# Performance work log

Measured on AMD Instinct MI355X. Metric: run time of the kernel, lower is better.

Reference implementation:

```python
import jax, jax.numpy as jnp
import numpy as np

N = 50000    # nodes
R = 3        # relations
E = 600000   # edges per relation
IN, HID, OUT = 128, 64, 64


def setup_inputs() -> dict:
    key = jax.random.key(0)
    k = jax.random.split(key, 5)
    x = jax.random.normal(k[0], (N, IN), dtype=jnp.float32)
    src = jax.random.randint(k[1], (R, E), 0, N, dtype=jnp.int32)
    dst = jax.random.randint(k[2], (R, E), 0, N, dtype=jnp.int32)
    # glorot-ish init like dgl.nn.GraphConv weight; bias init zeros
    W1 = jax.random.normal(k[3], (R, IN, HID), dtype=jnp.float32) * (IN ** -0.5)
    b1 = jnp.zeros((R, HID), dtype=jnp.float32)
    W2 = jax.random.normal(k[4], (R, HID, OUT), dtype=jnp.float32) * (HID ** -0.5)
    b2 = jnp.zeros((R, OUT), dtype=jnp.float32)
    return {"x": x, "W1": W1, "b1": b1, "W2": W2, "b2": b2, "src": src, "dst": dst}


def _graph_conv(x, src, dst, W, b):
    """dgl.nn.GraphConv with norm='both', single relation.
    x: [N, Fin]; src/dst: [E] int; W: [Fin, Fout]; b: [Fout].
    """
    n = x.shape[0]
    ones = jnp.ones(src.shape[0], dtype=x.dtype)
    out_deg = jax.ops.segment_sum(ones, src, num_segments=n)
    h = x * (jnp.maximum(out_deg, 1.0) ** -0.5)[:, None]   # src-side norm
    if W.shape[0] > W.shape[1]:
        # mult W first, then aggregate (fewer flops per edge)
        h = h @ W
        agg = jax.ops.segment_sum(h[src], dst, num_segments=n)  # [N, Fout]
    else:
        agg = jax.ops.segment_sum(h[src], dst, num_segments=n) @ W
    in_deg = jax.ops.segment_sum(ones, dst, num_segments=n)
    return agg * (jnp.maximum(in_deg, 1.0) ** -0.5)[:, None] + b


def _hetero_conv(x, src, dst, W, b):
    # HeteroGraphConv(aggregate='sum'): run each relation's GraphConv, sum results.
    per_rel = jax.vmap(_graph_conv, in_axes=(None, 0, 0, 0, 0))(x, src, dst, W, b)
    return per_rel.sum(axis=0)  # [N, Fout]


def reference(x, W1, b1, W2, b2, src, dst):
    h = jax.nn.relu(_hetero_conv(x, src, dst, W1, b1))
    return _hetero_conv(h, src, dst, W2, b2)
```

## Files before the change

kernel.cpp:

```cpp
#include <hip/hip_runtime.h>

#define NODES 50000
#define RELS  3
#define NEDGE 600000
#define FIN   128
#define FHID  64
#define FOUT  64
#define SEGS  (RELS * NODES)
#define NBLK  ((SEGS + 255) / 256)

#define HC     96
#define HCHUNK (NEDGE / HC)
#define HBYTES NODES
#define HWORDS (HBYTES / 4)

#define BS     250
#define NBUK   200
#define NBUKT  (RELS * NBUK)
#define CAPLOG 12
#define CAP    (1 << CAPLOG)
#define BCH    192
#define BCHUNK (NEDGE / BCH)

typedef _Float16 half8 __attribute__((ext_vector_type(8)));
typedef float   floatx4 __attribute__((ext_vector_type(4)));

__global__ __launch_bounds__(1024) void hist_kernel(const int* __restrict__ src,
                                                    const int* __restrict__ dst,
                                                    unsigned int* __restrict__ slab32,
                                                    int* __restrict__ bcur) {
    __shared__ unsigned int bins[HWORDS];
    int chunk = blockIdx.x, job = blockIdx.y;
    if (chunk == 0 && job == 0 && threadIdx.x < NBUKT) bcur[threadIdx.x] = 0;
    const int* arr = (job < 3 ? src + (size_t)job * NEDGE
                              : dst + (size_t)(job - 3) * NEDGE) + (size_t)chunk * HCHUNK;
    for (int w = threadIdx.x; w < HWORDS; w += 1024) bins[w] = 0u;
    __syncthreads();
    for (int i = threadIdx.x; i < HCHUNK; i += 1024) {
        int v = arr[i];
        atomicAdd(&bins[v >> 2], 1u << ((v & 3) * 8));
    }
    __syncthreads();
    unsigned int* out = slab32 + ((size_t)(job * HC + chunk)) * HWORDS;
    for (int w = threadIdx.x; w < HWORDS; w += 1024) out[w] = bins[w];
}

__global__ __launch_bounds__(512) void bucketize_kernel(const int* __restrict__ src,
                                                        const int* __restrict__ dst,
                                                        int* __restrict__ bcur,
                                                        unsigned int* __restrict__ rec) {
    __shared__ unsigned int stage[BCHUNK];
    __shared__ int bh[NBUK], bbase[NBUK], blc[NBUK];
    int chunk = blockIdx.x, r = blockIdx.y;
    for (int i = threadIdx.x; i < NBUK; i += 512) { bh[i] = 0; blc[i] = 0; }
    __syncthreads();
    size_t ebase = (size_t)r * NEDGE + (size_t)chunk * BCHUNK;
    for (int i = threadIdx.x; i < BCHUNK; i += 512) {
        int d = dst[ebase + i], s = src[ebase + i];
        int b = d / BS;
        int dl = d - b * BS;
        stage[i] = ((unsigned)s << 16) | ((unsigned)b << 8) | (unsigned)dl;
        atomicAdd(&bh[b], 1);
    }
    __syncthreads();
    for (int i = threadIdx.x; i < NBUK; i += 512)
        bbase[i] = atomicAdd(&bcur[r * NBUK + i], bh[i]);
    __syncthreads();
    for (int i = threadIdx.x; i < BCHUNK; i += 512) {
        unsigned u = stage[i];
        int b = (u >> 8) & 255;
        int slot = bbase[b] + atomicAdd(&blc[b], 1);
        rec[(((size_t)r * NBUK + b) << CAPLOG) + slot] = u;
    }
}

__global__ __launch_bounds__(256) void degnorm_kernel(const unsigned char* __restrict__ slab8,
                                                      int* __restrict__ idI,
                                                      float* __restrict__ outnorm,
                                                      float* __restrict__ innorm,
                                                      const float* __restrict__ W1,
                                                      const float* __restrict__ W2,
                                                      _Float16* __restrict__ W1t,
                                                      _Float16* __restrict__ W2t) {
    int gid = blockIdx.x * 256 + threadIdx.x;
    if (gid < 6 * NODES) {
        int j = gid / NODES, b = gid - j * NODES;
        size_t base = (size_t)j * HC * HBYTES + b;
        int sum = 0;
#pragma unroll 4
        for (int c = 0; c < HC; ++c) sum += slab8[base + (size_t)c * HBYTES];
        float nrm = rsqrtf(fmaxf((float)sum, 1.0f));
        if (j < 3) {
            outnorm[j * NODES + b] = nrm;
        } else {
            idI[(j - 3) * NODES + b] = sum;
            innorm[(j - 3) * NODES + b] = nrm;
        }
        return;
    }
    int g2 = gid - 6 * NODES;
    if (g2 < RELS * FIN * FHID) {
        int r = g2 / (FIN * FHID);
        int rem = g2 - r * FIN * FHID;
        int k = rem / FHID, j = rem - k * FHID;
        W1t[((size_t)r * FHID + j) * FIN + k] = (_Float16)W1[g2];
        return;
    }
    int g3 = g2 - RELS * FIN * FHID;
    if (g3 < RELS * FHID * FOUT) {
        int r = g3 / (FHID * FOUT);
        int rem = g3 - r * FHID * FOUT;
        int k = rem / FOUT, j = rem - k * FOUT;
        W2t[((size_t)r * FOUT + j) * FHID + k] = (_Float16)W2[g3];
    }
}

__global__ __launch_bounds__(256) void scan_sums_kernel(const int* __restrict__ idI,
                                                        int* __restrict__ partials) {
    __shared__ int s[256];
    int i = blockIdx.x * 256 + threadIdx.x;
    s[threadIdx.x] = (i < SEGS) ? idI[i] : 0;
    __syncthreads();
    for (int off = 128; off > 0; off >>= 1) {
        if (threadIdx.x < off) s[threadIdx.x] += s[threadIdx.x + off];
        __syncthreads();
    }
    if (threadIdx.x == 0) partials[blockIdx.x] = s[0];
}

__global__ __launch_bounds__(256) void scan_write_kernel(const int* __restrict__ idI,
                                                         const int* __restrict__ partials,
                                                         int* __restrict__ offs) {
    __shared__ int sp[1024];
    __shared__ int s[256];
    int tid = threadIdx.x;
    for (int i = tid; i < 1024; i += 256) sp[i] = (i < NBLK) ? partials[i] : 0;
    __syncthreads();
    for (int off = 1; off < 1024; off <<= 1) {
        int v[4];
#pragma unroll
        for (int k = 0; k < 4; ++k) { int i = tid + k * 256; v[k] = (i >= off) ? sp[i - off] : 0; }
        __syncthreads();
#pragma unroll
        for (int k = 0; k < 4; ++k) sp[tid + k * 256] += v[k];
        __syncthreads();
    }
    int bpre = (blockIdx.x == 0) ? 0 : sp[blockIdx.x - 1];
    int i = blockIdx.x * 256 + tid;
    int v = (i < SEGS) ? idI[i] : 0;
    s[tid] = v;
    __syncthreads();
    for (int off = 1; off < 256; off <<= 1) {
        int t = s[tid];
        int add = (tid >= off) ? s[tid - off] : 0;
        __syncthreads();
        s[tid] = t + add;
        __syncthreads();
    }
    if (i < SEGS) offs[i] = bpre + (s[tid] - v);
}

__global__ __launch_bounds__(512) void fillbkt_kernel(const unsigned int* __restrict__ rec,
                                                      const int* __restrict__ bcur,
                                                      const int* __restrict__ offs,
                                                      unsigned short* __restrict__ edge_src) {
    __shared__ int obase[BS];
    __shared__ int lcur[BS];
    int b = blockIdx.x, r = blockIdx.y;
    int segbase = r * NODES + b * BS;
    for (int i = threadIdx.x; i < BS; i += 512) {
        obase[i] = offs[segbase + i];
        lcur[i] = 0;
    }
    __syncthreads();
    int n = bcur[r * NBUK + b];
    const unsigned int* rb = rec + (((size_t)r * NBUK + b) << CAPLOG);
    for (int i = threadIdx.x; i < n; i += 512) {
        unsigned u = rb[i];
        int dl = u & 255;
        int pos = obase[dl] + atomicAdd(&lcur[dl], 1);
        edge_src[pos] = (unsigned short)(u >> 16);
    }
}

__global__ __launch_bounds__(256, 4) void gemm1_kernel(const float* __restrict__ x,
                                                       const _Float16* __restrict__ W1t,
                                                       const float* __restrict__ outnorm,
                                                       _Float16* __restrict__ h) {
    int lane = threadIdx.x & 63;
    int wv   = threadIdx.x >> 6;
    int m = lane & 15, quad = lane >> 4;
    int n0 = (blockIdx.x * 4 + wv) * 16;
    if (n0 + 16 > NODES) n0 = NODES - 16;
    const float* xrow = x + (size_t)(n0 + m) * FIN + quad * 8;

    floatx4 acc[12];
#pragma unroll
    for (int t = 0; t < 12; ++t) acc[t] = (floatx4){0.f, 0.f, 0.f, 0.f};

#pragma unroll 1
    for (int ks = 0; ks < 4; ++ks) {
        float4 xa = *(const float4*)(xrow + ks * 32);
        float4 xb = *(const float4*)(xrow + ks * 32 + 4);
        half8 a;
        a[0] = (_Float16)xa.x; a[1] = (_Float16)xa.y;
        a[2] = (_Float16)xa.z; a[3] = (_Float16)xa.w;
        a[4] = (_Float16)xb.x; a[5] = (_Float16)xb.y;
        a[6] = (_Float16)xb.z; a[7] = (_Float16)xb.w;
#pragma unroll
        for (int jt = 0; jt < 12; ++jt) {
            const _Float16* bp = W1t + ((size_t)jt * 16 + m) * FIN + ks * 32 + quad * 8;
            half8 b = *(const half8*)bp;
            acc[jt] = __builtin_amdgcn_mfma_f32_16x16x32_f16(a, b, acc[jt], 0, 0, 0);
        }
    }

#pragma unroll
    for (int jt = 0; jt < 12; ++jt) {
        int r = jt >> 2;
        int j = (jt & 3) * 16 + m;
        _Float16* hb = h + (size_t)r * NODES * FHID;
        const float* on = outnorm + r * NODES;
#pragma unroll
        for (int reg = 0; reg < 4; ++reg) {
            int node = n0 + quad * 4 + reg;
            hb[(size_t)node * FHID + j] = (_Float16)(acc[jt][reg] * on[node]);
        }
    }
}

__device__ __forceinline__ void seg_sum8(const _Float16* __restrict__ hb,
                                         const unsigned short* __restrict__ es,
                                         int o, int c, int q, float* __restrict__ s) {
#pragma unroll
    for (int i = 0; i < 8; ++i) s[i] = 0.f;
    int t = 0;
    for (; t + 4 <= c; t += 4) {
        int i0 = es[o + t], i1 = es[o + t + 1], i2 = es[o + t + 2], i3 = es[o + t + 3];
        half8 v0 = *(const half8*)(hb + (size_t)i0 * FHID + q * 8);
        half8 v1 = *(const half8*)(hb + (size_t)i1 * FHID + q * 8);
        half8 v2 = *(const half8*)(hb + (size_t)i2 * FHID + q * 8);
        half8 v3 = *(const half8*)(hb + (size_t)i3 * FHID + q * 8);
#pragma unroll
        for (int i = 0; i < 8; ++i) {
            s[i] += (float)v0[i];
            s[i] += (float)v1[i];
            s[i] += (float)v2[i];
            s[i] += (float)v3[i];
        }
    }
    if (t + 2 <= c) {
        int i0 = es[o + t], i1 = es[o + t + 1];
        half8 v0 = *(const half8*)(hb + (size_t)i0 * FHID + q * 8);
        half8 v1 = *(const half8*)(hb + (size_t)i1 * FHID + q * 8);
#pragma unroll
        for (int i = 0; i < 8; ++i) {
            s[i] += (float)v0[i];
            s[i] += (float)v1[i];
        }
        t += 2;
    }
    if (t < c) {
        int i0 = es[o + t];
        half8 v0 = *(const half8*)(hb + (size_t)i0 * FHID + q * 8);
#pragma unroll
        for (int i = 0; i < 8; ++i) s[i] += (float)v0[i];
    }
}

__global__ __launch_bounds__(256) void gather1_kernel(const _Float16* __restrict__ h,
                                                      const unsigned short* __restrict__ es,
                                                      const int* __restrict__ offs,
                                                      const int* __restrict__ cnt,
                                                      const float* __restrict__ innorm,
                                                      const float* __restrict__ b1,
                                                      _Float16* __restrict__ B) {
    int lane = threadIdx.x & 63;
    int wv   = threadIdx.x >> 6;
    int w    = blockIdx.x * 4 + wv;
    if (w * 8 >= NODES) return;
    int q    = lane & 7;
    int e8   = lane >> 3;
    int d    = w * 8 + e8;
    int c0 = cnt[d], c1 = cnt[NODES + d], c2 = cnt[2 * NODES + d];
    int o0 = offs[d], o1 = offs[NODES + d], o2 = offs[2 * NODES + d];
    float w0 = innorm[d], w1 = innorm[NODES + d], w2 = innorm[2 * NODES + d];

    float tot[8], s[8];
    seg_sum8(h, es, o0, c0, q, s);
#pragma unroll
    for (int i = 0; i < 8; ++i) tot[i] = w0 * s[i];
    seg_sum8(h + (size_t)NODES * FHID, es, o1, c1, q, s);
#pragma unroll
    for (int i = 0; i < 8; ++i) tot[i] = fmaf(w1, s[i], tot[i]);
    seg_sum8(h + 2 * (size_t)NODES * FHID, es, o2, c2, q, s);
#pragma unroll
    for (int i = 0; i < 8; ++i) tot[i] = fmaf(w2, s[i], tot[i]);

    half8 o8;
#pragma unroll
    for (int i = 0; i < 8; ++i) {
        int j = q * 8 + i;
        float bs = b1[j] + b1[FHID + j] + b1[2 * FHID + j];
        o8[i] = (_Float16)fmaxf(tot[i] + bs, 0.f);
    }
    *(half8*)(B + (size_t)d * FHID + q * 8) = o8;
}

__global__ __launch_bounds__(256) void gather2_kernel(const _Float16* __restrict__ h1,
                                                      const unsigned short* __restrict__ es,
                                                      const int* __restrict__ offs,
                                                      const int* __restrict__ cnt,
                                                      const float* __restrict__ outnorm,
                                                      const float* __restrict__ innorm,
                                                      _Float16* __restrict__ A2) {
    int lane = threadIdx.x & 63;
    int wv   = threadIdx.x >> 6;
    int w    = blockIdx.x * 4 + wv;
    int s0   = w * 8;
    if (s0 >= SEGS) return;
    int q    = lane & 7;
    int e8   = lane >> 3;
    int seg  = s0 + e8;
    int o = offs[seg], c = cnt[seg];
    const float* on = outnorm + (s0 / NODES) * NODES;

    float tot[8];
#pragma unroll
    for (int i = 0; i < 8; ++i) tot[i] = 0.f;
    int t = 0;
    for (; t + 4 <= c; t += 4) {
        int i0 = es[o + t], i1 = es[o + t + 1], i2 = es[o + t + 2], i3 = es[o + t + 3];
        float w0 = on[i0], w1 = on[i1], w2 = on[i2], w3 = on[i3];
        half8 v0 = *(const half8*)(h1 + (size_t)i0 * FHID + q * 8);
        half8 v1 = *(const half8*)(h1 + (size_t)i1 * FHID + q * 8);
        half8 v2 = *(const half8*)(h1 + (size_t)i2 * FHID + q * 8);
        half8 v3 = *(const half8*)(h1 + (size_t)i3 * FHID + q * 8);
#pragma unroll
        for (int i = 0; i < 8; ++i) {
            tot[i] = fmaf(w0, (float)v0[i], tot[i]);
            tot[i] = fmaf(w1, (float)v1[i], tot[i]);
            tot[i] = fmaf(w2, (float)v2[i], tot[i]);
            tot[i] = fmaf(w3, (float)v3[i], tot[i]);
        }
    }
    if (t + 2 <= c) {
        int i0 = es[o + t], i1 = es[o + t + 1];
        float w0 = on[i0], w1 = on[i1];
        half8 v0 = *(const half8*)(h1 + (size_t)i0 * FHID + q * 8);
        half8 v1 = *(const half8*)(h1 + (size_t)i1 * FHID + q * 8);
#pragma unroll
        for (int i = 0; i < 8; ++i) {
            tot[i] = fmaf(w0, (float)v0[i], tot[i]);
            tot[i] = fmaf(w1, (float)v1[i], tot[i]);
        }
        t += 2;
    }
    if (t < c) {
        int i0 = es[o + t];
        float w0 = on[i0];
        half8 v0 = *(const half8*)(h1 + (size_t)i0 * FHID + q * 8);
#pragma unroll
        for (int i = 0; i < 8; ++i) tot[i] = fmaf(w0, (float)v0[i], tot[i]);
    }

    float inr = innorm[seg];
    half8 o8;
#pragma unroll
    for (int i = 0; i < 8; ++i) o8[i] = (_Float16)(inr * tot[i]);
    *(half8*)(A2 + (size_t)seg * FHID + q * 8) = o8;
}

__global__ __launch_bounds__(256, 4) void out_kernel(const _Float16* __restrict__ A2,
                                                     const _Float16* __restrict__ W2t,
                                                     const float* __restrict__ b2,
                                                     float* __restrict__ out) {
    int lane = threadIdx.x & 63;
    int wv   = threadIdx.x >> 6;
    int m = lane & 15, quad = lane >> 4;
    int n0 = (blockIdx.x * 4 + wv) * 16;
    if (n0 + 16 > NODES) n0 = NODES - 16;

    floatx4 acc[4];
#pragma unroll
    for (int t = 0; t < 4; ++t) acc[t] = (floatx4){0.f, 0.f, 0.f, 0.f};

#pragma unroll 1
    for (int kk = 0; kk < 6; ++kk) {
        int r = kk >> 1, kb = (kk & 1) * 32;
        const _Float16* ap = A2 + ((size_t)r * NODES + n0 + m) * FHID + kb + quad * 8;
        half8 a = *(const half8*)ap;
#pragma unroll
        for (int jt = 0; jt < 4; ++jt) {
            const _Float16* bp = W2t + ((size_t)(r * FOUT + jt * 16 + m)) * FHID + kb + quad * 8;
            half8 b = *(const half8*)bp;
            acc[jt] = __builtin_amdgcn_mfma_f32_16x16x32_f16(a, b, acc[jt], 0, 0, 0);
        }
    }

#pragma unroll
    for (int jt = 0; jt < 4; ++jt) {
        int j = jt * 16 + m;
        float bs = b2[j] + b2[FOUT + j] + b2[2 * FOUT + j];
#pragma unroll
        for (int reg = 0; reg < 4; ++reg) {
            int node = n0 + quad * 4 + reg;
            out[(size_t)node * FOUT + j] = acc[jt][reg] + bs;
        }
    }
}

extern "C" void kernel_launch(void* const* d_in, const int* in_sizes, int n_in,
                              void* d_out, int out_size, void* d_ws, size_t ws_size,
                              hipStream_t stream) {
    const float* x   = (const float*)d_in[0];
    const float* W1  = (const float*)d_in[1];
    const float* b1  = (const float*)d_in[2];
    const float* W2  = (const float*)d_in[3];
    const float* b2  = (const float*)d_in[4];
    const int*   src = (const int*)d_in[5];
    const int*   dst = (const int*)d_in[6];
    float* out = (float*)d_out;

    int*   idI      = (int*)d_ws;
    int*   offs     = idI + SEGS;
    int*   partials = offs + SEGS;
    int*   bcur     = partials + 1024;
    unsigned short* edge_src = (unsigned short*)(bcur + 1024);
    float* outnorm  = (float*)(edge_src + (size_t)RELS * NEDGE);
    float* innorm   = outnorm + SEGS;
    _Float16* W1t   = (_Float16*)(innorm + SEGS);
    _Float16* W2t   = W1t + (size_t)RELS * FHID * FIN;
    _Float16* h     = W2t + (size_t)RELS * FHID * FOUT;
    _Float16* B     = h + (size_t)SEGS * FHID;
    _Float16* A2    = B + (size_t)NODES * FHID;
    unsigned int*  slab32 = (unsigned int*)h;
    unsigned char* slab8  = (unsigned char*)h;
    unsigned int*  rec    = (unsigned int*)(slab8 + (size_t)6 * HC * HBYTES);

    const int GW = ((NODES / 16) + 4) / 4;

    hist_kernel<<<dim3(HC, 6), 1024, 0, stream>>>(src, dst, slab32, bcur);
    bucketize_kernel<<<dim3(BCH, RELS), 512, 0, stream>>>(src, dst, bcur, rec);
    degnorm_kernel<<<(6 * NODES + RELS * FIN * FHID + RELS * FHID * FOUT + 255) / 256,
                     256, 0, stream>>>(slab8, idI, outnorm, innorm, W1, W2, W1t, W2t);
    scan_sums_kernel<<<NBLK, 256, 0, stream>>>(idI, partials);
    scan_write_kernel<<<NBLK, 256, 0, stream>>>(idI, partials, offs);
    fillbkt_kernel<<<dim3(NBUK, RELS), 512, 0, stream>>>(rec, bcur, offs, edge_src);

    gemm1_kernel<<<GW, 256, 0, stream>>>(x, W1t, outnorm, h);
    gather1_kernel<<<(NODES / 8 + 3) / 4, 256, 0, stream>>>(h, edge_src, offs, idI, innorm, b1, B);

    gather2_kernel<<<(SEGS / 8 + 3) / 4, 256, 0, stream>>>(B, edge_src, offs, idI, outnorm, innorm, A2);
    out_kernel<<<GW, 256, 0, stream>>>(A2, W2t, b2, out);
}
```

Before: 250.2 us.

## Replace slab histogram with bucket-based in-degree and global-atomic out-degree

Removes the separate per-chunk byte-histogram pass over src/dst and the slab reduction in degnorm. Out-degrees are now counted with global atomics inside the bucketize kernel, and in-degrees are counted per bucket from the already-bucketized records in a small shared-memory kernel. This drops a full read of both edge arrays and the large slab write and read-back. In exchange it adds global atomic contention on source nodes and one more small kernel, plus an init kernel to zero the counters.

Result: slower. 321.4 us (+28.5%).

```diff
diff --git a/kernel.cpp b/kernel.cpp
--- a/kernel.cpp
+++ b/kernel.cpp
@@ -9,11 +9,6 @@
 #define SEGS  (RELS * NODES)
 #define NBLK  ((SEGS + 255) / 256)
 
-#define HC     96
-#define HCHUNK (NEDGE / HC)
-#define HBYTES NODES
-#define HWORDS (HBYTES / 4)
-
 #define BS     250
 #define NBUK   200
 #define NBUKT  (RELS * NBUK)
@@ -25,29 +20,39 @@
 typedef _Float16 half8 __attribute__((ext_vector_type(8)));
 typedef float   floatx4 __attribute__((ext_vector_type(4)));
 
-__global__ __launch_bounds__(1024) void hist_kernel(const int* __restrict__ src,
-                                                    const int* __restrict__ dst,
-                                                    unsigned int* __restrict__ slab32,
-                                                    int* __restrict__ bcur) {
-    __shared__ unsigned int bins[HWORDS];
-    int chunk = blockIdx.x, job = blockIdx.y;
-    if (chunk == 0 && job == 0 && threadIdx.x < NBUKT) bcur[threadIdx.x] = 0;
-    const int* arr = (job < 3 ? src + (size_t)job * NEDGE
-                              : dst + (size_t)(job - 3) * NEDGE) + (size_t)chunk * HCHUNK;
-    for (int w = threadIdx.x; w < HWORDS; w += 1024) bins[w] = 0u;
-    __syncthreads();
-    for (int i = threadIdx.x; i < HCHUNK; i += 1024) {
-        int v = arr[i];
-        atomicAdd(&bins[v >> 2], 1u << ((v & 3) * 8));
-    }
-    __syncthreads();
-    unsigned int* out = slab32 + ((size_t)(job * HC + chunk)) * HWORDS;
-    for (int w = threadIdx.x; w < HWORDS; w += 1024) out[w] = bins[w];
+__global__ __launch_bounds__(256) void init_kernel(int* __restrict__ odeg,
+                                                   int* __restrict__ bcur,
+                                                   const float* __restrict__ W1,
+                                                   const float* __restrict__ W2,
+                                                   _Float16* __restrict__ W1t,
+                                                   _Float16* __restrict__ W2t) {
+    int gid = blockIdx.x * 256 + threadIdx.x;
+    if (gid < SEGS) {
+        odeg[gid] = 0;
+        if (gid < NBUKT) bcur[gid] = 0;
+        return;
+    }
+    int g2 = gid - SEGS;
+    if (g2 < RELS * FIN * FHID) {
+        int r = g2 / (FIN * FHID);
+        int rem = g2 - r * FIN * FHID;
+        int k = rem / FHID, j = rem - k * FHID;
+        W1t[((size_t)r * FHID + j) * FIN + k] = (_Float16)W1[g2];
+        return;
+    }
+    int g3 = g2 - RELS * FIN * FHID;
+    if (g3 < RELS * FHID * FOUT) {
+        int r = g3 / (FHID * FOUT);
+        int rem = g3 - r * FHID * FOUT;
+        int k = rem / FOUT, j = rem - k * FOUT;
+        W2t[((size_t)r * FOUT + j) * FHID + k] = (_Float16)W2[g3];
+    }
 }
 
 __global__ __launch_bounds__(512) void bucketize_kernel(const int* __restrict__ src,
                                                         const int* __restrict__ dst,
                                                         int* __restrict__ bcur,
+                                                        int* __restrict__ odeg,
                                                         unsigned int* __restrict__ rec) {
     __shared__ unsigned int stage[BCHUNK];
     __shared__ int bh[NBUK], bbase[NBUK], blc[NBUK];
@@ -55,12 +60,14 @@
     for (int i = threadIdx.x; i < NBUK; i += 512) { bh[i] = 0; blc[i] = 0; }
     __syncthreads();
     size_t ebase = (size_t)r * NEDGE + (size_t)chunk * BCHUNK;
+    int* od = odeg + r * NODES;
     for (int i = threadIdx.x; i < BCHUNK; i += 512) {
         int d = dst[ebase + i], s = src[ebase + i];
         int b = d / BS;
         int dl = d - b * BS;
         stage[i] = ((unsigned)s << 16) | ((unsigned)b << 8) | (unsigned)dl;
         atomicAdd(&bh[b], 1);
+        atomicAdd(&od[s], 1);
     }
     __syncthreads();
     for (int i = threadIdx.x; i < NBUK; i += 512)
@@ -74,44 +81,26 @@
     }
 }
 
-__global__ __launch_bounds__(256) void degnorm_kernel(const unsigned char* __restrict__ slab8,
-                                                      int* __restrict__ idI,
-                                                      float* __restrict__ outnorm,
-                                                      float* __restrict__ innorm,
-                                                      const float* __restrict__ W1,
-                                                      const float* __restrict__ W2,
-                                                      _Float16* __restrict__ W1t,
-                                                      _Float16* __restrict__ W2t) {
-    int gid = blockIdx.x * 256 + threadIdx.x;
-    if (gid < 6 * NODES) {
-        int j = gid / NODES, b = gid - j * NODES;
-        size_t base = (size_t)j * HC * HBYTES + b;
-        int sum = 0;
-#pragma unroll 4
-        for (int c = 0; c < HC; ++c) sum += slab8[base + (size_t)c * HBYTES];
-        float nrm = rsqrtf(fmaxf((float)sum, 1.0f));
-        if (j < 3) {
-            outnorm[j * NODES + b] = nrm;
-        } else {
-            idI[(j - 3) * NODES + b] = sum;
-            innorm[(j - 3) * NODES + b] = nrm;
-        }
-        return;
-    }
-    int g2 = gid - 6 * NODES;
-    if (g2 < RELS * FIN * FHID) {
-        int r = g2 / (FIN * FHID);
-        int rem = g2 - r * FIN * FHID;
-        int k = rem / FHID, j = rem - k * FHID;
-        W1t[((size_t)r * FHID + j) * FIN + k] = (_Float16)W1[g2];
-        return;
-    }
-    int g3 = g2 - RELS * FIN * FHID;
-    if (g3 < RELS * FHID * FOUT) {
-        int r = g3 / (FHID * FOUT);
-        int rem = g3 - r * FHID * FOUT;
-        int k = rem / FOUT, j = rem - k * FOUT;
-        W2t[((size_t)r * FOUT + j) * FHID + k] = (_Float16)W2[g3];
+__global__ __launch_bounds__(256) void degbkt_kernel(const unsigned int* __restrict__ rec,
+                                                     const int* __restrict__ bcur,
+                                                     const int* __restrict__ odeg,
+                                                     int* __restrict__ idI,
+                                                     float* __restrict__ innorm,
+                                                     float* __restrict__ outnorm) {
+    __shared__ int cnt[BS];
+    int b = blockIdx.x, r = blockIdx.y;
+    for (int i = threadIdx.x; i < BS; i += 256) cnt[i] = 0;
+    __syncthreads();
+    int n = bcur[r * NBUK + b];
+    const unsigned int* rb = rec + (((size_t)r * NBUK + b) << CAPLOG);
+    for (int i = threadIdx.x; i < n; i += 256) atomicAdd(&cnt[rb[i] & 255], 1);
+    __syncthreads();
+    int segbase = r * NODES + b * BS;
+    for (int i = threadIdx.x; i < BS; i += 256) {
+        int c = cnt[i];
+        idI[segbase + i] = c;
+        innorm[segbase + i] = rsqrtf(fmaxf((float)c, 1.0f));
+        outnorm[segbase + i] = rsqrtf(fmaxf((float)odeg[segbase + i], 1.0f));
     }
 }
 
@@ -426,7 +415,8 @@
     int*   offs     = idI + SEGS;
     int*   partials = offs + SEGS;
     int*   bcur     = partials + 1024;
-    unsigned short* edge_src = (unsigned short*)(bcur + 1024);
+    int*   odeg     = bcur + 1024;
+    unsigned short* edge_src = (unsigned short*)(odeg + SEGS);
     float* outnorm  = (float*)(edge_src + (size_t)RELS * NEDGE);
     float* innorm   = outnorm + SEGS;
     _Float16* W1t   = (_Float16*)(innorm + SEGS);
@@ -434,16 +424,14 @@
     _Float16* h     = W2t + (size_t)RELS * FHID * FOUT;
     _Float16* B     = h + (size_t)SEGS * FHID;
     _Float16* A2    = B + (size_t)NODES * FHID;
-    unsigned int*  slab32 = (unsigned int*)h;
-    unsigned char* slab8  = (unsigned char*)h;
-    unsigned int*  rec    = (unsigned int*)(slab8 + (size_t)6 * HC * HBYTES);
+    unsigned int*  rec = (unsigned int*)h;
 
     const int GW = ((NODES / 16) + 4) / 4;
 
-    hist_kernel<<<dim3(HC, 6), 1024, 0, stream>>>(src, dst, slab32, bcur);
-    bucketize_kernel<<<dim3(BCH, RELS), 512, 0, stream>>>(src, dst, bcur, rec);
-    degnorm_kernel<<<(6 * NODES + RELS * FIN * FHID + RELS * FHID * FOUT + 255) / 256,
-                     256, 0, stream>>>(slab8, idI, outnorm, innorm, W1, W2, W1t, W2t);
+    init_kernel<<<(SEGS + RELS * FIN * FHID + RELS * FHID * FOUT + 255) / 256,
+                  256, 0, stream>>>(odeg, bcur, W1, W2, W1t, W2t);
+    bucketize_kernel<<<dim3(BCH, RELS), 512, 0, stream>>>(src, dst, bcur, odeg, rec);
+    degbkt_kernel<<<dim3(NBUK, RELS), 256, 0, stream>>>(rec, bcur, odeg, idI, innorm, outnorm);
     scan_sums_kernel<<<NBLK, 256, 0, stream>>>(idI, partials);
     scan_write_kernel<<<NBLK, 256, 0, stream>>>(idI, partials, offs);
     fillbkt_kernel<<<dim3(NBUK, RELS), 512, 0, stream>>>(rec, bcur, offs, edge_src);
```
